# Performance work log

Measured on AMD Instinct MI355X. Metric: run time of the kernel, lower is better.

## Reference

```python
import jax, jax.numpy as jnp
import numpy as np

K = 16                 # hardcoded k in KL_divergence default
TYPICAL_CRLB = 0.15 * 100 / 10   # = 1.5, sigma used in KL divergence


def setup_inputs() -> dict:
    key = jax.random.key(0)
    k1, k2 = jax.random.split(key)
    N = 8192
    ch1 = jax.random.normal(k1, (N, 2), dtype=jnp.float32)
    ch2 = jax.random.normal(k2, (N, 2), dtype=jnp.float32)
    # Polynomial layer parameters, exactly as in __init__ (identity-ish map)
    M1 = jnp.array([[0.0, 0.0], [1.0, 0.0]], dtype=jnp.float32)
    M2 = jnp.array([[0.0, 1.0], [0.0, 0.0]], dtype=jnp.float32)
    return {"ch1": ch1, "ch2": ch2, "M1": M1, "M2": M2}


def _polynomial(x, M1, M2):
    # out[:,0] = sum_ij M1[i,j] * x1^i * x2^j ; out[:,1] analog with M2 (m=2)
    x1, x2 = x[:, 0], x[:, 1]
    pi = jnp.stack([jnp.ones_like(x1), x1], axis=1)          # [N,2] -> x1^i
    pj = jnp.stack([jnp.ones_like(x2), x2], axis=1)          # [N,2] -> x2^j
    B = pi[:, :, None] * pj[:, None, :]                      # [N,2,2] basis x1^i*x2^j
    y1 = jnp.einsum('nij,ij->n', B, M1)
    y2 = jnp.einsum('nij,ij->n', B, M2)
    return jnp.stack([y1, y2], axis=1)                       # [N,2]


def reference(ch1, ch2, M1, M2):
    N = ch1.shape[0]
    ch2m = _polynomial(ch2, M1, M2)

    # --- KNN ---
    diff = ch1[None, :, :] - ch2m[:, None, :]                # [N2, N1, 2]
    distances = diff * diff                                  # squared per-coord dists
    abs_distances = jnp.sum(distances, axis=2)               # [N2, N1]
    # top_k of negated transposed distances: for each ch1 point, k nearest ch2m
    _, idx = jax.lax.top_k(-abs_distances.T, K)              # [N1, K] indices into ch2 axis
    # Faithful reproduction of the original index construction:
    # idx is flattened row-major ([N,K]); indx1 flattens a [K,N] arange-broadcast,
    # so the second coordinate at flat position t is t % N.
    flat_a = idx.reshape(-1)                                 # [N*K] indexes axis 0 (ch2)
    flat_b = jnp.tile(jnp.arange(N), K)                      # [N*K] indexes axis 1 (ch1)
    knn = distances[flat_a, flat_b].reshape(K, N, 2)         # [K, N, 2]

    # --- KL divergence ---
    sigma2 = TYPICAL_CRLB
    D_KL = 0.5 * jnp.sum(knn / (sigma2 ** 2), axis=2)        # [K, N]

    # --- Rel entropy ---
    expD = jnp.sum(jnp.exp(-D_KL), axis=0) / N               # [N]
    mask = expD != 0.0                                       # tf boolean_mask of nonzeros
    safe = jnp.where(mask, expD, 1.0)
    return -jnp.sum(jnp.where(mask, jnp.log(safe), 0.0))
```

## Files before the change

### kernel.cpp

```cpp
#include <hip/hip_runtime.h>
#include <math.h>
#include <stdint.h>

#define K_NN 16
#define NPTS 8192
#define HALF (NPTS / 2)
#define STEPS (HALF / 256)
#define WPB 16

__global__ __launch_bounds__(1024) void k1_knn(const float* __restrict__ ch1,
                                               const float* __restrict__ ch2,
                                               const float* __restrict__ M1,
                                               const float* __restrict__ M2,
                                               int* __restrict__ midx,
                                               float* __restrict__ out) {
    __shared__ float2 sh[HALF];

    const int tid  = threadIdx.x;
    const int lane = tid & 63;
    const int w    = tid >> 6;
    const int qg   = blockIdx.x * WPB + w;

    if (blockIdx.x == 0 && tid == 0) out[0] = 0.0f;

    const float q0 = ch1[2 * qg + 0];
    const float q1 = ch1[2 * qg + 1];

    const float a0 = M1[0], a1 = M1[1], a2 = M1[2], a3 = M1[3];
    const float b0 = M2[0], b1 = M2[1], b2 = M2[2], b3 = M2[3];

    const float4* __restrict__ g4 = (const float4*)ch2;

    unsigned key = 0xFFFFFFFFu;
    unsigned kth = 0xFFFFFFFFu;
    unsigned thr = 0xFFFFFFFFu;

#define INSERT_EVENT(NDV, CIDX)                                                \
    {                                                                          \
        int l = __ffsll(m) - 1;                                                \
        unsigned snd = (unsigned)__builtin_amdgcn_readlane(                    \
            __float_as_int(NDV), l);                                           \
        unsigned snk = (snd & 0xFFFFE000u) | (unsigned)(sbase + (CIDX));       \
        if (snk < kth) {                                                       \
            unsigned up = (unsigned)__builtin_amdgcn_update_dpp(               \
                0, (int)key, 0x111, 0xF, 0xF, false);           \
            bool c1 = snk < key;                                               \
            unsigned nv = (snk < up) ? up : snk;                               \
            key = c1 ? nv : key;                                               \
            kth = (unsigned)__builtin_amdgcn_readlane((int)key, 15);           \
            thr = kth | 0x1FFFu;                                               \
        }                                                                      \
        m &= m - 1;                                                            \
        m &= __ballot(__float_as_uint(NDV) <= thr);                            \
    }

    for (int pass = 0; pass < 2; ++pass) {
        __syncthreads();
#pragma unroll
        for (int e = 0; e < (HALF / 2) / 1024; ++e) {
            float4 v = g4[pass * (HALF / 2) + e * 1024 + tid];
            float px0 = a0 + a1 * v.y + v.x * (a2 + a3 * v.y);
            float py0 = b0 + b1 * v.y + v.x * (b2 + b3 * v.y);
            float px1 = a0 + a1 * v.w + v.z * (a2 + a3 * v.w);
            float py1 = b0 + b1 * v.w + v.z * (b2 + b3 * v.w);
            ((float4*)sh)[e * 1024 + tid] = make_float4(px0, py0, px1, py1);
        }
        __syncthreads();

        const float4* s4 = (const float4*)sh;
        float4 ca = s4[lane];
        float4 cb = s4[64 + lane];

        for (int t = 0; t < STEPS; ++t) {
            int tn = (t + 1) & (STEPS - 1);
            float4 na = s4[tn * 128 + lane];
            float4 nb = s4[tn * 128 + 64 + lane];

            const int sbase = pass * HALF + t * 256;

            float dx0 = q0 - ca.x, dy0 = q1 - ca.y;
            float dx1 = q0 - ca.z, dy1 = q1 - ca.w;
            float dx2 = q0 - cb.x, dy2 = q1 - cb.y;
            float dx3 = q0 - cb.z, dy3 = q1 - cb.w;
            float nd0 = dx0 * dx0 + dy0 * dy0;
            float nd1 = dx1 * dx1 + dy1 * dy1;
            float nd2 = dx2 * dx2 + dy2 * dy2;
            float nd3 = dx3 * dx3 + dy3 * dy3;

            unsigned long long m;
            m = __ballot(__float_as_uint(nd0) <= thr);
            while (m) INSERT_EVENT(nd0, 2 * l)
            m = __ballot(__float_as_uint(nd1) <= thr);
            while (m) INSERT_EVENT(nd1, 2 * l + 1)
            m = __ballot(__float_as_uint(nd2) <= thr);
            while (m) INSERT_EVENT(nd2, 128 + 2 * l)
            m = __ballot(__float_as_uint(nd3) <= thr);
            while (m) INSERT_EVENT(nd3, 128 + 2 * l + 1)

            ca = na;
            cb = nb;
        }
    }
#undef INSERT_EVENT

    if (lane < K_NN)
        midx[qg * K_NN + lane] = (int)(key & 0x1FFFu);
}

__global__ __launch_bounds__(1024) void k3_final(const float* __restrict__ ch1,
                                                 const float* __restrict__ ch2,
                                                 const float* __restrict__ M1,
                                                 const float* __restrict__ M2,
                                                 const int* __restrict__ midx,
                                                 float* __restrict__ out, int N) {
    const float a0 = M1[0], a1 = M1[1], a2 = M1[2], a3 = M1[3];
    const float b0 = M2[0], b1 = M2[1], b2 = M2[2], b3 = M2[3];

    int t = blockIdx.x * 1024 + threadIdx.x;
    int n = t >> 4;
    int k = t & 15;
    int g = n >> 4;
    int r = n & 15;

    int j = k * (N / K_NN) + g;
    int a = midx[j * K_NN + r];
    float2 cp = ((const float2*)ch2)[a];
    float cx = a0 + a1 * cp.y + cp.x * (a2 + a3 * cp.y);
    float cy = b0 + b1 * cp.y + cp.x * (b2 + b3 * cp.y);
    float dx = ch1[2 * n + 0] - cx;
    float dy = ch1[2 * n + 1] - cy;
    float term = expf(-(dx * dx + dy * dy) * (1.0f / 4.5f));

#pragma unroll
    for (int off = 8; off; off >>= 1) term += __shfl_down(term, off, 16);

    float v = 0.0f;
    if (k == 0) {
        float expD = term / (float)N;
        v = (expD != 0.0f) ? logf(expD) : 0.0f;
    }
#pragma unroll
    for (int off = 32; off; off >>= 1) v += __shfl_down(v, off, 64);

    __shared__ float red[16];
    int lane = threadIdx.x & 63;
    int wv = threadIdx.x >> 6;
    if (lane == 0) red[wv] = v;
    __syncthreads();
    if (threadIdx.x == 0) {
        float s = 0.0f;
#pragma unroll
        for (int i = 0; i < 16; ++i) s += red[i];
        atomicAdd(out, -s);
    }
}

extern "C" void kernel_launch(void* const* d_in, const int* in_sizes, int n_in,
                              void* d_out, int out_size, void* d_ws, size_t ws_size,
                              hipStream_t stream) {
    const float* ch1 = (const float*)d_in[0];
    const float* ch2 = (const float*)d_in[1];
    const float* M1  = (const float*)d_in[2];
    const float* M2  = (const float*)d_in[3];
    float* out = (float*)d_out;
    const int N = in_sizes[0] / 2;

    int* midx = (int*)d_ws;

    k1_knn<<<N / WPB, 1024, 0, stream>>>(ch1, ch2, M1, M2, midx, out);

    k3_final<<<(N * K_NN) / 1024, 1024, 0, stream>>>(ch1, ch2, M1, M2, midx, out, N);
}
```

Measured before the change: 99.78 us.

## Batch KNN insert ballots per step and seed threshold from first tile

```diff
diff --git a/kernel.cpp b/kernel.cpp
--- a/kernel.cpp
+++ b/kernel.cpp
@@ -32,26 +32,18 @@
     const float4* __restrict__ g4 = (const float4*)ch2;
 
     unsigned key = 0xFFFFFFFFu;
-    unsigned kth = 0xFFFFFFFFu;
     unsigned thr = 0xFFFFFFFFu;
 
-#define INSERT_EVENT(NDV, CIDX)                                                \
-    {                                                                          \
-        int l = __ffsll(m) - 1;                                                \
-        unsigned snd = (unsigned)__builtin_amdgcn_readlane(                    \
-            __float_as_int(NDV), l);                                           \
-        unsigned snk = (snd & 0xFFFFE000u) | (unsigned)(sbase + (CIDX));       \
-        if (snk < kth) {                                                       \
-            unsigned up = (unsigned)__builtin_amdgcn_update_dpp(               \
-                0, (int)key, 0x111, 0xF, 0xF, false);           \
-            bool c1 = snk < key;                                               \
-            unsigned nv = (snk < up) ? up : snk;                               \
-            key = c1 ? nv : key;                                               \
-            kth = (unsigned)__builtin_amdgcn_readlane((int)key, 15);           \
-            thr = kth | 0x1FFFu;                                               \
-        }                                                                      \
-        m &= m - 1;                                                            \
-        m &= __ballot(__float_as_uint(NDV) <= thr);                            \
+#define INSERT_EVENTS(MV, NKV)                                                 \
+    while (MV) {                                                               \
+        int l = __ffsll(MV) - 1;                                               \
+        MV &= MV - 1;                                                          \
+        unsigned snk = (unsigned)__builtin_amdgcn_readlane((int)(NKV), l);     \
+        unsigned up = (unsigned)__builtin_amdgcn_update_dpp(                   \
+            0, (int)key, 0x111, 0xF, 0xF, false);               \
+        bool c1 = snk < key;                                                   \
+        unsigned nv = (snk < up) ? up : snk;                                   \
+        key = c1 ? nv : key;                                                   \
     }
 
     for (int pass = 0; pass < 2; ++pass) {
@@ -76,32 +68,51 @@
             float4 na = s4[tn * 128 + lane];
             float4 nb = s4[tn * 128 + 64 + lane];
 
-            const int sbase = pass * HALF + t * 256;
+            const int base = pass * HALF + t * 256 + 2 * lane;
 
             float dx0 = q0 - ca.x, dy0 = q1 - ca.y;
             float dx1 = q0 - ca.z, dy1 = q1 - ca.w;
             float dx2 = q0 - cb.x, dy2 = q1 - cb.y;
             float dx3 = q0 - cb.z, dy3 = q1 - cb.w;
-            float nd0 = dx0 * dx0 + dy0 * dy0;
-            float nd1 = dx1 * dx1 + dy1 * dy1;
-            float nd2 = dx2 * dx2 + dy2 * dy2;
-            float nd3 = dx3 * dx3 + dy3 * dy3;
+            unsigned u0 = __float_as_uint(dx0 * dx0 + dy0 * dy0);
+            unsigned u1 = __float_as_uint(dx1 * dx1 + dy1 * dy1);
+            unsigned u2 = __float_as_uint(dx2 * dx2 + dy2 * dy2);
+            unsigned u3 = __float_as_uint(dx3 * dx3 + dy3 * dy3);
 
-            unsigned long long m;
-            m = __ballot(__float_as_uint(nd0) <= thr);
-            while (m) INSERT_EVENT(nd0, 2 * l)
-            m = __ballot(__float_as_uint(nd1) <= thr);
-            while (m) INSERT_EVENT(nd1, 2 * l + 1)
-            m = __ballot(__float_as_uint(nd2) <= thr);
-            while (m) INSERT_EVENT(nd2, 128 + 2 * l)
-            m = __ballot(__float_as_uint(nd3) <= thr);
-            while (m) INSERT_EVENT(nd3, 128 + 2 * l + 1)
+            if (pass == 0 && t == 0) {
+                unsigned mn = min(min(u0, u1), min(u2, u3));
+                mn = min(mn, (unsigned)__shfl_xor((int)mn, 1, 64));
+                mn = min(mn, (unsigned)__shfl_xor((int)mn, 2, 64));
+                unsigned mx = mn;
+                mx = max(mx, (unsigned)__shfl_xor((int)mx, 4, 64));
+                mx = max(mx, (unsigned)__shfl_xor((int)mx, 8, 64));
+                mx = max(mx, (unsigned)__shfl_xor((int)mx, 16, 64));
+                mx = max(mx, (unsigned)__shfl_xor((int)mx, 32, 64));
+                thr = mx | 0x1FFFu;
+            }
+
+            unsigned nk0 = (u0 & 0xFFFFE000u) | (unsigned)base;
+            unsigned nk1 = (u1 & 0xFFFFE000u) | (unsigned)(base + 1);
+            unsigned nk2 = (u2 & 0xFFFFE000u) | (unsigned)(base + 128);
+            unsigned nk3 = (u3 & 0xFFFFE000u) | (unsigned)(base + 129);
+
+            unsigned long long m0 = __ballot(u0 <= thr);
+            unsigned long long m1 = __ballot(u1 <= thr);
+            unsigned long long m2 = __ballot(u2 <= thr);
+            unsigned long long m3 = __ballot(u3 <= thr);
+
+            INSERT_EVENTS(m0, nk0)
+            INSERT_EVENTS(m1, nk1)
+            INSERT_EVENTS(m2, nk2)
+            INSERT_EVENTS(m3, nk3)
+
+            thr = (unsigned)__builtin_amdgcn_readlane((int)key, 15) | 0x1FFFu;
 
             ca = na;
             cb = nb;
         }
     }
-#undef INSERT_EVENT
+#undef INSERT_EVENTS
 
     if (lane < K_NN)
         midx[qg * K_NN + lane] = (int)(key & 0x1FFFu);
```

Measured after the change: 90.93 us. 8.9% less time.
